# Kernel tuning notes

Hardware: AMD Instinct MI355X
Metric: run time of the kernel (lower is better)

Reference implementation:

```python
import jax, jax.numpy as jnp
import numpy as np

EXP_ORDER = 2  # matches init_kwargs exp_order
N_FEAT = 8
Q_DIM = 1
BATCH = 262144
T_EXPANDED = 164  # n + C(n+1,2) + C(n+2,3) for n=8, degrees 1..3
N_OUT = 8


def taylor_expand(x, exp_order):
    """Faithful vectorized version of the nested multiply/concat loop.

    x: [B, n, q]. Builds all monomials of degree 1..exp_order+1 using the same
    recursion as the TF code: at each order, for each j, multiply x_j with the
    previous-order block starting at Id[j], then append. The q-loop in the
    original is replaced by broadcasting over the q axis (identical math).
    """
    n = x.shape[1]
    Id = list(range(n))  # start index of x_j's block in the previous-order terms
    epd = x
    for _ in range(exp_order):
        L = epd.shape[1]  # slice end Id[n-1]+1 always equals current length
        blocks = []
        new_Id = []
        offset = L
        for j in range(n):
            blk = x[:, j:j + 1, :] * epd[:, Id[j]:L, :]  # [B, L-Id[j], q]
            new_Id.append(offset)
            offset += blk.shape[1]
            blocks.append(blk)
        epd = jnp.concatenate([epd] + blocks, axis=1)
        Id = new_Id
    return epd


def setup_inputs() -> dict:
    key = jax.random.key(0)
    k1, k2, k3 = jax.random.split(key, 3)
    x = jax.random.normal(k1, (BATCH, N_FEAT, Q_DIM), dtype=jnp.float32)
    # 'dl' init: uniform(-1/sqrt(fan), 1/sqrt(fan)) with fan = weights_shape[0]
    dl_scale = 1.0 / np.sqrt(N_OUT)
    W = jax.random.uniform(k2, (N_OUT, T_EXPANDED), minval=-dl_scale,
                           maxval=dl_scale, dtype=jnp.float32)
    # 'uniform' bias init: U(-0.2, 0.2), shape [out, 1]
    b = jax.random.uniform(k3, (N_OUT, 1), minval=-0.2, maxval=0.2,
                           dtype=jnp.float32)
    return {"x": x, "W": W, "b": b}


def reference(x, W, b):
    # cp_type == 'none': pass-through of the input
    epd = taylor_expand(x, EXP_ORDER)          # [B, T, q]
    out = jnp.einsum('ot,btq->boq', W, epd) + b[None]  # [B, out, q]
    # act_type == 'relu'
    return jax.nn.relu(out)
```

## Files before the change

kernel.cpp:

```cpp
#include <hip/hip_runtime.h>
#include <hip/hip_bf16.h>
#include <string.h>


static constexpr int TEXP = 164;
static constexpr int NOUT = 8;
static constexpr int NMFMA = 11;
static constexpr int HALF = 88;

using f32x16 = __attribute__((ext_vector_type(16))) float;
using short8 = __attribute__((ext_vector_type(8))) short;

constexpr int rowstart2(int j) { return j * 8 - j * (j - 1) / 2; }
constexpr int start3(int j) {
  int s = 44;
  for (int jp = 0; jp < j; ++jp) s += (8 - jp) * (9 - jp) / 2;
  return s;
}
struct D3 { int j, p; };
constexpr D3 d3idx(int M) {
  int j = 0;
  while (start3(j + 1) <= M) ++j;
  int q = M - start3(j);
  int a = j;
  while (q >= (8 - a)) { q -= (8 - a); ++a; }
  int b = a + q;
  return { j, rowstart2(a) + (b - a) };
}

template <int M>
__device__ __forceinline__ float mono(const float (&xv)[8], const float (&d2)[36]) {
  if constexpr (M < 8) {
    return xv[M];
  } else if constexpr (M < 44) {
    return d2[M - 8];
  } else {
    constexpr D3 t = d3idx(M);
    return xv[t.j] * d2[t.p];
  }
}

__device__ __forceinline__ short bf16bits(float v) {
  __hip_bfloat16 h = __float2bfloat16(v);
  short s;
  memcpy(&s, &h, 2);
  return s;
}

template <int C>
__device__ __forceinline__ void do_slot(const float (&xv)[8], const float (&d2)[36],
                                        bool hi, short8& bv) {
  float v0 = mono<C>(xv, d2);
  float v1;
  if constexpr (HALF + C < TEXP) v1 = mono<HALF + C>(xv, d2);
  else v1 = 0.0f;
  float v = hi ? v1 : v0;
  bv[C & 7] = bf16bits(v);
}

template <int I>
__device__ __forceinline__ void slot8(const float (&xv)[8], const float (&d2)[36],
                                      bool hi, short8& bv) {
  do_slot<8 * I + 0>(xv, d2, hi, bv);
  do_slot<8 * I + 1>(xv, d2, hi, bv);
  do_slot<8 * I + 2>(xv, d2, hi, bv);
  do_slot<8 * I + 3>(xv, d2, hi, bv);
  do_slot<8 * I + 4>(xv, d2, hi, bv);
  do_slot<8 * I + 5>(xv, d2, hi, bv);
  do_slot<8 * I + 6>(xv, d2, hi, bv);
  do_slot<8 * I + 7>(xv, d2, hi, bv);
}

template <int I>
struct MfmaStep {
  static __device__ __forceinline__ void run(const float (&xv)[8], const float (&d2)[36],
                                             bool hi, const short8 (&af)[NMFMA],
                                             f32x16& acc) {
    short8 bv;
    slot8<I>(xv, d2, hi, bv);
    acc = __builtin_amdgcn_mfma_f32_32x32x16_bf16(af[I], bv, acc, 0, 0, 0);
    MfmaStep<I + 1>::run(xv, d2, hi, af, acc);
  }
};
template <>
struct MfmaStep<NMFMA> {
  static __device__ __forceinline__ void run(const float (&)[8], const float (&)[36],
                                             bool, const short8 (&)[NMFMA], f32x16&) {}
};

__global__ void prep_w(const float* __restrict__ W, unsigned short* __restrict__ wp) {
  for (int idx = threadIdx.x + blockIdx.x * blockDim.x; idx < NMFMA * 64 * 8;
       idx += blockDim.x * gridDim.x) {
    int j = idx & 7;
    int lane = (idx >> 3) & 63;
    int i = idx >> 9;
    int row = lane & 31, h = lane >> 5;
    int m = HALF * h + 8 * i + j;
    float v = (row < NOUT && m < TEXP) ? W[row * TEXP + m] : 0.0f;
    union { float f; unsigned int u; } c; c.f = v;
    unsigned int u = c.u;
    wp[idx] = (unsigned short)((u + 0x7fffu + ((u >> 16) & 1u)) >> 16);
  }
}

__global__ __launch_bounds__(256) void taylor_mfma(
    const float* __restrict__ x, const float* __restrict__ b,
    const unsigned short* __restrict__ wp, float* __restrict__ out, int ngroups) {
  const int lane = (int)(threadIdx.x & 63);
  const bool hi = lane >= 32;
  const int col = lane & 31;
  const int h4 = hi ? 4 : 0;

  short8 afrag[NMFMA];
#pragma unroll
  for (int i = 0; i < NMFMA; ++i)
    afrag[i] = *reinterpret_cast<const short8*>(wp + (i * 64 + lane) * 8);

  const float4 bv4 = *reinterpret_cast<const float4*>(b + h4);

  const int wave = (int)((blockIdx.x * blockDim.x + threadIdx.x) >> 6);
  const int nw = (int)((gridDim.x * blockDim.x) >> 6);

  for (int g = wave; g < ngroups; g += nw) {
    const int elem = g * 32 + col;
    float4 xa = reinterpret_cast<const float4*>(x)[elem * 2 + 0];
    float4 xb = reinterpret_cast<const float4*>(x)[elem * 2 + 1];
    float xv[8] = {xa.x, xa.y, xa.z, xa.w, xb.x, xb.y, xb.z, xb.w};

    float d2[36];
#pragma unroll
    for (int j = 0; j < 8; ++j) {
#pragma unroll
      for (int k = j; k < 8; ++k) {
        d2[rowstart2(j) + (k - j)] = xv[j] * xv[k];
      }
    }

    f32x16 acc;
#pragma unroll
    for (int r = 0; r < 16; ++r) acc[r] = 0.0f;

    MfmaStep<0>::run(xv, d2, hi, afrag, acc);

    float4 o;
    o.x = fmaxf(acc[0] + bv4.x, 0.0f);
    o.y = fmaxf(acc[1] + bv4.y, 0.0f);
    o.z = fmaxf(acc[2] + bv4.z, 0.0f);
    o.w = fmaxf(acc[3] + bv4.w, 0.0f);
    reinterpret_cast<float4*>(out)[elem * 2 + (hi ? 1 : 0)] = o;
  }
}

extern "C" void kernel_launch(void* const* d_in, const int* in_sizes, int n_in,
                              void* d_out, int out_size, void* d_ws, size_t ws_size,
                              hipStream_t stream) {
  const float* x = (const float*)d_in[0];
  const float* W = (const float*)d_in[1];
  const float* b = (const float*)d_in[2];
  float* out = (float*)d_out;
  unsigned short* wp = (unsigned short*)d_ws;

  int n = in_sizes[0] / 8;
  int ngroups = n / 32;

  prep_w<<<8, 256, 0, stream>>>(W, wp);
  taylor_mfma<<<1024, 256, 0, stream>>>(x, b, wp, out, ngroups);
}
```

Measured before the change: 17.64 us.

## Fold weight bf16 packing into main kernel and launch one wave per group

Drops the separate prep_w kernel. Each wave now reads W straight from global memory, converts it to bf16 and builds its MFMA A-fragments in registers, which removes a kernel launch and the workspace round-trip. The persistent grid-stride loop is replaced by a grid sized to the problem, with one 32-element group per wave. The trade-off is that the W load and conversion are repeated in every wave instead of being amortised over many groups, and there are more blocks to schedule.

```diff
diff --git a/kernel.cpp b/kernel.cpp
--- a/kernel.cpp
+++ b/kernel.cpp
@@ -88,67 +88,82 @@
                                              bool, const short8 (&)[NMFMA], f32x16&) {}
 };
 
-__global__ void prep_w(const float* __restrict__ W, unsigned short* __restrict__ wp) {
-  for (int idx = threadIdx.x + blockIdx.x * blockDim.x; idx < NMFMA * 64 * 8;
-       idx += blockDim.x * gridDim.x) {
-    int j = idx & 7;
-    int lane = (idx >> 3) & 63;
-    int i = idx >> 9;
-    int row = lane & 31, h = lane >> 5;
-    int m = HALF * h + 8 * i + j;
-    float v = (row < NOUT && m < TEXP) ? W[row * TEXP + m] : 0.0f;
-    union { float f; unsigned int u; } c; c.f = v;
-    unsigned int u = c.u;
-    wp[idx] = (unsigned short)((u + 0x7fffu + ((u >> 16) & 1u)) >> 16);
-  }
-}
-
 __global__ __launch_bounds__(256) void taylor_mfma(
-    const float* __restrict__ x, const float* __restrict__ b,
-    const unsigned short* __restrict__ wp, float* __restrict__ out, int ngroups) {
+    const float* __restrict__ x, const float* __restrict__ W,
+    const float* __restrict__ b, float* __restrict__ out, int ngroups) {
   const int lane = (int)(threadIdx.x & 63);
   const bool hi = lane >= 32;
+  const int h = hi ? 1 : 0;
   const int col = lane & 31;
-  const int h4 = hi ? 4 : 0;
+
+  const int row = lane & 7;
+  const float* wr = W + row * TEXP;
+  const int mbase = h * HALF;
 
   short8 afrag[NMFMA];
 #pragma unroll
-  for (int i = 0; i < NMFMA; ++i)
-    afrag[i] = *reinterpret_cast<const short8*>(wp + (i * 64 + lane) * 8);
+  for (int i = 0; i < 9; ++i) {
+    float4 fa = *reinterpret_cast<const float4*>(wr + mbase + 8 * i);
+    float4 fb = *reinterpret_cast<const float4*>(wr + mbase + 8 * i + 4);
+    short8 f;
+    f[0] = bf16bits(fa.x); f[1] = bf16bits(fa.y);
+    f[2] = bf16bits(fa.z); f[3] = bf16bits(fa.w);
+    f[4] = bf16bits(fb.x); f[5] = bf16bits(fb.y);
+    f[6] = bf16bits(fb.z); f[7] = bf16bits(fb.w);
+    afrag[i] = f;
+  }
+  {
+    float4 fa = *reinterpret_cast<const float4*>(wr + mbase + 72);
+    float4 fb = *reinterpret_cast<const float4*>(wr + (hi ? 156 : 76));
+    short8 f;
+    f[0] = bf16bits(fa.x); f[1] = bf16bits(fa.y);
+    f[2] = bf16bits(fa.z); f[3] = bf16bits(fa.w);
+    f[4] = bf16bits(hi ? 0.0f : fb.x); f[5] = bf16bits(hi ? 0.0f : fb.y);
+    f[6] = bf16bits(hi ? 0.0f : fb.z); f[7] = bf16bits(hi ? 0.0f : fb.w);
+    afrag[9] = f;
+  }
+  {
+    float4 fa = *reinterpret_cast<const float4*>(wr + 80);
+    float4 fb = *reinterpret_cast<const float4*>(wr + 84);
+    short8 f;
+    f[0] = bf16bits(hi ? 0.0f : fa.x); f[1] = bf16bits(hi ? 0.0f : fa.y);
+    f[2] = bf16bits(hi ? 0.0f : fa.z); f[3] = bf16bits(hi ? 0.0f : fa.w);
+    f[4] = bf16bits(hi ? 0.0f : fb.x); f[5] = bf16bits(hi ? 0.0f : fb.y);
+    f[6] = bf16bits(hi ? 0.0f : fb.z); f[7] = bf16bits(hi ? 0.0f : fb.w);
+    afrag[10] = f;
+  }
 
-  const float4 bv4 = *reinterpret_cast<const float4*>(b + h4);
+  const float4 bv4 = *reinterpret_cast<const float4*>(b + 4 * h);
 
-  const int wave = (int)((blockIdx.x * blockDim.x + threadIdx.x) >> 6);
-  const int nw = (int)((gridDim.x * blockDim.x) >> 6);
+  const int g = (int)((blockIdx.x * blockDim.x + threadIdx.x) >> 6);
+  if (g >= ngroups) return;
 
-  for (int g = wave; g < ngroups; g += nw) {
-    const int elem = g * 32 + col;
-    float4 xa = reinterpret_cast<const float4*>(x)[elem * 2 + 0];
-    float4 xb = reinterpret_cast<const float4*>(x)[elem * 2 + 1];
-    float xv[8] = {xa.x, xa.y, xa.z, xa.w, xb.x, xb.y, xb.z, xb.w};
+  const int elem = g * 32 + col;
+  float4 xa = reinterpret_cast<const float4*>(x)[elem * 2 + 0];
+  float4 xb = reinterpret_cast<const float4*>(x)[elem * 2 + 1];
+  float xv[8] = {xa.x, xa.y, xa.z, xa.w, xb.x, xb.y, xb.z, xb.w};
 
-    float d2[36];
+  float d2[36];
 #pragma unroll
-    for (int j = 0; j < 8; ++j) {
+  for (int j = 0; j < 8; ++j) {
 #pragma unroll
-      for (int k = j; k < 8; ++k) {
-        d2[rowstart2(j) + (k - j)] = xv[j] * xv[k];
-      }
+    for (int k = j; k < 8; ++k) {
+      d2[rowstart2(j) + (k - j)] = xv[j] * xv[k];
     }
+  }
 
-    f32x16 acc;
+  f32x16 acc;
 #pragma unroll
-    for (int r = 0; r < 16; ++r) acc[r] = 0.0f;
+  for (int r = 0; r < 16; ++r) acc[r] = 0.0f;
 
-    MfmaStep<0>::run(xv, d2, hi, afrag, acc);
+  MfmaStep<0>::run(xv, d2, hi, afrag, acc);
 
-    float4 o;
-    o.x = fmaxf(acc[0] + bv4.x, 0.0f);
-    o.y = fmaxf(acc[1] + bv4.y, 0.0f);
-    o.z = fmaxf(acc[2] + bv4.z, 0.0f);
-    o.w = fmaxf(acc[3] + bv4.w, 0.0f);
-    reinterpret_cast<float4*>(out)[elem * 2 + (hi ? 1 : 0)] = o;
-  }
+  float4 o;
+  o.x = fmaxf(acc[0] + bv4.x, 0.0f);
+  o.y = fmaxf(acc[1] + bv4.y, 0.0f);
+  o.z = fmaxf(acc[2] + bv4.z, 0.0f);
+  o.w = fmaxf(acc[3] + bv4.w, 0.0f);
+  *reinterpret_cast<float4*>(out + elem * 8 + 4 * h) = o;
 }
 
 extern "C" void kernel_launch(void* const* d_in, const int* in_sizes, int n_in,
@@ -158,11 +173,10 @@
   const float* W = (const float*)d_in[1];
   const float* b = (const float*)d_in[2];
   float* out = (float*)d_out;
-  unsigned short* wp = (unsigned short*)d_ws;
 
   int n = in_sizes[0] / 8;
   int ngroups = n / 32;
-
-  prep_w<<<8, 256, 0, stream>>>(W, wp);
-  taylor_mfma<<<1024, 256, 0, stream>>>(x, b, wp, out, ngroups);
+  int waves_per_block = 4;
+  int blocks = (ngroups + waves_per_block - 1) / waves_per_block;
+  taylor_mfma<<<blocks, 256, 0, stream>>>(x, W, b, out, ngroups);
 }
```

New measurement: 18.21 us. 3.2% more time.

## Launch one wave per group and stream weight fragments per MFMA step

Applied to the files above, without the earlier changes.

Drops the grid-stride loop over groups. The kernel now launches one wave per 32-element group, so there are ngroups/4 blocks, and each wave processes exactly one group. Instead of keeping all 11 bf16 weight fragments in registers, each MFMA step prefetches the next fragment from global memory (L2/L1), with sched_barriers enforcing the order. Launch bounds are raised to request higher occupancy. The aim is to cut register pressure and raise latency hiding. In exchange, every wave reloads the weights and there is more block-launch overhead and extra memory traffic.

```diff
diff --git a/kernel.cpp b/kernel.cpp
--- a/kernel.cpp
+++ b/kernel.cpp
@@ -74,18 +74,18 @@
 template <int I>
 struct MfmaStep {
   static __device__ __forceinline__ void run(const float (&xv)[8], const float (&d2)[36],
-                                             bool hi, const short8 (&af)[NMFMA],
-                                             f32x16& acc) {
+                                             bool hi, const unsigned short* __restrict__ wpl,
+                                             short8 af_cur, f32x16& acc) {
+    short8 af_next;
+    if constexpr (I + 1 < NMFMA)
+      af_next = *reinterpret_cast<const short8*>(wpl + (I + 1) * 64 * 8);
     short8 bv;
     slot8<I>(xv, d2, hi, bv);
-    acc = __builtin_amdgcn_mfma_f32_32x32x16_bf16(af[I], bv, acc, 0, 0, 0);
-    MfmaStep<I + 1>::run(xv, d2, hi, af, acc);
+    acc = __builtin_amdgcn_mfma_f32_32x32x16_bf16(af_cur, bv, acc, 0, 0, 0);
+    __builtin_amdgcn_sched_barrier(0);
+    if constexpr (I + 1 < NMFMA)
+      MfmaStep<I + 1>::run(xv, d2, hi, wpl, af_next, acc);
   }
-};
-template <>
-struct MfmaStep<NMFMA> {
-  static __device__ __forceinline__ void run(const float (&)[8], const float (&)[36],
-                                             bool, const short8 (&)[NMFMA], f32x16&) {}
 };
 
 __global__ void prep_w(const float* __restrict__ W, unsigned short* __restrict__ wp) {
@@ -103,52 +103,48 @@
   }
 }
 
-__global__ __launch_bounds__(256) void taylor_mfma(
+__global__ __launch_bounds__(256, 4) void taylor_mfma(
     const float* __restrict__ x, const float* __restrict__ b,
     const unsigned short* __restrict__ wp, float* __restrict__ out, int ngroups) {
   const int lane = (int)(threadIdx.x & 63);
   const bool hi = lane >= 32;
+  const int h = hi ? 1 : 0;
   const int col = lane & 31;
-  const int h4 = hi ? 4 : 0;
 
-  short8 afrag[NMFMA];
+  const unsigned short* wpl = wp + lane * 8;
+  short8 af0 = *reinterpret_cast<const short8*>(wpl);
+
+  const float4 bv4 = *reinterpret_cast<const float4*>(b + 4 * h);
+
+  const int g = (int)((blockIdx.x * blockDim.x + threadIdx.x) >> 6);
+  if (g >= ngroups) return;
+
+  const int elem = g * 32 + col;
+  float4 xa = reinterpret_cast<const float4*>(x)[elem * 2 + 0];
+  float4 xb = reinterpret_cast<const float4*>(x)[elem * 2 + 1];
+  float xv[8] = {xa.x, xa.y, xa.z, xa.w, xb.x, xb.y, xb.z, xb.w};
+
+  float d2[36];
 #pragma unroll
-  for (int i = 0; i < NMFMA; ++i)
-    afrag[i] = *reinterpret_cast<const short8*>(wp + (i * 64 + lane) * 8);
+  for (int j = 0; j < 8; ++j) {
+#pragma unroll
+    for (int k = j; k < 8; ++k) {
+      d2[rowstart2(j) + (k - j)] = xv[j] * xv[k];
+    }
+  }
 
-  const float4 bv4 = *reinterpret_cast<const float4*>(b + h4);
+  f32x16 acc;
+#pragma unroll
+  for (int r = 0; r < 16; ++r) acc[r] = 0.0f;
 
-  const int wave = (int)((blockIdx.x * blockDim.x + threadIdx.x) >> 6);
-  const int nw = (int)((gridDim.x * blockDim.x) >> 6);
+  MfmaStep<0>::run(xv, d2, hi, wpl, af0, acc);
 
-  for (int g = wave; g < ngroups; g += nw) {
-    const int elem = g * 32 + col;
-    float4 xa = reinterpret_cast<const float4*>(x)[elem * 2 + 0];
-    float4 xb = reinterpret_cast<const float4*>(x)[elem * 2 + 1];
-    float xv[8] = {xa.x, xa.y, xa.z, xa.w, xb.x, xb.y, xb.z, xb.w};
-
-    float d2[36];
-#pragma unroll
-    for (int j = 0; j < 8; ++j) {
-#pragma unroll
-      for (int k = j; k < 8; ++k) {
-        d2[rowstart2(j) + (k - j)] = xv[j] * xv[k];
-      }
-    }
-
-    f32x16 acc;
-#pragma unroll
-    for (int r = 0; r < 16; ++r) acc[r] = 0.0f;
-
-    MfmaStep<0>::run(xv, d2, hi, afrag, acc);
-
-    float4 o;
-    o.x = fmaxf(acc[0] + bv4.x, 0.0f);
-    o.y = fmaxf(acc[1] + bv4.y, 0.0f);
-    o.z = fmaxf(acc[2] + bv4.z, 0.0f);
-    o.w = fmaxf(acc[3] + bv4.w, 0.0f);
-    reinterpret_cast<float4*>(out)[elem * 2 + (hi ? 1 : 0)] = o;
-  }
+  float4 o;
+  o.x = fmaxf(acc[0] + bv4.x, 0.0f);
+  o.y = fmaxf(acc[1] + bv4.y, 0.0f);
+  o.z = fmaxf(acc[2] + bv4.z, 0.0f);
+  o.w = fmaxf(acc[3] + bv4.w, 0.0f);
+  *reinterpret_cast<float4*>(out + elem * 8 + 4 * h) = o;
 }
 
 extern "C" void kernel_launch(void* const* d_in, const int* in_sizes, int n_in,
@@ -162,7 +158,8 @@
 
   int n = in_sizes[0] / 8;
   int ngroups = n / 32;
+  int blocks = ngroups / 4;
 
   prep_w<<<8, 256, 0, stream>>>(W, wp);
-  taylor_mfma<<<1024, 256, 0, stream>>>(x, b, wp, out, ngroups);
+  taylor_mfma<<<blocks, 256, 0, stream>>>(x, b, wp, out, ngroups);
 }
```

New measurement: 17.26 us. 1.02x faster.
